# Kernel tuning notes

Measured on AMD Instinct MI355X. Metric: run time of the kernel, lower is better.

## Reference

```python
import jax, jax.numpy as jnp
import numpy as np

B, IN_DIM, K, D = 8192, 1024, 2048, 256
TAU = 1.0
BN_EPS = 1e-5


def setup_inputs() -> dict:
    key = jax.random.key(0)
    ks = jax.random.split(key, 4)
    x = jax.random.normal(ks[0], (B, IN_DIM), dtype=jnp.float32)
    u = jax.random.uniform(ks[1], (B, K), dtype=jnp.float32)  # uniform for gumbel noise
    W = jax.random.normal(ks[2], (IN_DIM, D), dtype=jnp.float32) * 0.02
    b = jnp.zeros((D,), dtype=jnp.float32)
    gamma = jnp.ones((D,), dtype=jnp.float32)
    beta = jnp.zeros((D,), dtype=jnp.float32)
    E = jax.random.normal(ks[3], (K, D), dtype=jnp.float32)  # nn.Embedding default N(0,1)
    return {"x": x, "u": u, "W": W, "b": b, "gamma": gamma, "beta": beta, "E": E}


def reference(x, u, W, b, gamma, beta, E):
    # classifier + BatchNorm1d (training mode: batch stats, biased variance)
    h = x @ W + b                                   # [B, D]
    mu = jnp.mean(h, axis=0)
    var = jnp.var(h, axis=0)
    h = (h - mu) * jax.lax.rsqrt(var + BN_EPS) * gamma + beta
    # negative squared euclidean distance via ||h||^2 - 2 h.E^T + ||e||^2 (GEMM form,
    # avoids materializing [B, K, D])
    h2 = jnp.sum(h * h, axis=-1, keepdims=True)     # [B, 1]
    e2 = jnp.sum(E * E, axis=-1)                    # [K]
    logits = -(h2 - 2.0 * (h @ E.T) + e2)           # [B, K]
    # gumbel-softmax (soft) with tau
    g = -jnp.log(-jnp.log(u + 1e-10) + 1e-10)
    assignments = jax.nn.softmax((logits + g) / TAU, axis=-1)  # [B, K]
    z = assignments @ E                             # [B, D]
    probs = jax.nn.softmax(logits, axis=-1)
    return probs, z
```

## Files before the change

### kernel.cpp

```cpp
#include <hip/hip_runtime.h>
#include <math.h>

#define B_SZ 8192
#define IN_DIM 1024
#define K_CB 2048
#define D_SZ 256
#define BN_EPS 1e-5f

typedef _Float16 f16;
typedef _Float16 f16x8 __attribute__((ext_vector_type(8)));
typedef _Float16 f16x4 __attribute__((ext_vector_type(4)));
typedef float    f32x4 __attribute__((ext_vector_type(4)));

#define GLOAD_LDS16(g, l) __builtin_amdgcn_global_load_lds(                      \
    (const __attribute__((address_space(1))) unsigned int*)(g),                  \
    (__attribute__((address_space(3))) unsigned int*)(l), 16, 0, 0)

template<int BM, int BN, int BK, int EPI, bool A32>
__global__ __launch_bounds__(256) void gemm_mfma(
    const void* __restrict__ Aptr, int lda,
    const f16* __restrict__ Bptr, int ldb,
    void* __restrict__ Cptr, int ldc, int Kdim,
    const float* __restrict__ bias)
{
    constexpr int G    = BK / 8;
    constexpr int MASK = G - 1;
    constexpr int WM = BM / 2, WN = BN / 2;
    constexpr int FM = WM / 16, FN = WN / 16;
    constexpr int CH_A = BM * G;
    constexpr int CH_B = BN * G;

    __shared__ char lds[(BM + BN) * BK * 2];
    char* As = lds;
    char* Bs = lds + BM * BK * 2;

    const int tid  = threadIdx.x;
    const int w    = tid >> 6, lane = tid & 63;
    const int wm   = w >> 1,   wn   = w & 1;
    const int row0 = blockIdx.x * BM;
    const int col0 = blockIdx.y * BN;

    f32x4 acc[FM][FN] = {};

    for (int k0 = 0; k0 < Kdim; k0 += BK) {
        #pragma unroll
        for (int i = 0; i < CH_B / 256; ++i) {
            const int base = (i * 4 + w) * 64;
            const int s = base + lane;
            const int r = s / G, c = s % G;
            const f16* src = Bptr + (size_t)(col0 + r) * ldb + k0 + ((c ^ (r & MASK)) * 8);
            GLOAD_LDS16(src, Bs + base * 16);
        }
        if (!A32) {
            #pragma unroll
            for (int i = 0; i < CH_A / 256; ++i) {
                const int base = (i * 4 + w) * 64;
                const int s = base + lane;
                const int r = s / G, c = s % G;
                const f16* src = (const f16*)Aptr + (size_t)(row0 + r) * lda + k0 + ((c ^ (r & MASK)) * 8);
                GLOAD_LDS16(src, As + base * 16);
            }
        } else {
            #pragma unroll
            for (int i = 0; i < CH_A / 256; ++i) {
                const int s = i * 256 + tid;
                const int r = s / G, c = s % G;
                const float* src = (const float*)Aptr + (size_t)(row0 + r) * lda + k0 + c * 8;
                const float4 v0 = ((const float4*)src)[0];
                const float4 v1 = ((const float4*)src)[1];
                f16x8 d;
                d[0] = (f16)v0.x; d[1] = (f16)v0.y; d[2] = (f16)v0.z; d[3] = (f16)v0.w;
                d[4] = (f16)v1.x; d[5] = (f16)v1.y; d[6] = (f16)v1.z; d[7] = (f16)v1.w;
                *(f16x8*)(As + (r * G + (c ^ (r & MASK))) * 16) = d;
            }
        }
        __syncthreads();

        #pragma unroll
        for (int kk = 0; kk < BK / 32; ++kk) {
            f16x8 af[FM], bf[FN];
            #pragma unroll
            for (int m = 0; m < FM; ++m) {
                const int r = wm * WM + m * 16 + (lane & 15);
                const int g = (kk * 4 + (lane >> 4)) ^ (r & MASK);
                af[m] = *(const f16x8*)(As + r * (BK * 2) + g * 16);
            }
            #pragma unroll
            for (int n = 0; n < FN; ++n) {
                const int r = wn * WN + n * 16 + (lane & 15);
                const int g = (kk * 4 + (lane >> 4)) ^ (r & MASK);
                bf[n] = *(const f16x8*)(Bs + r * (BK * 2) + g * 16);
            }
            #pragma unroll
            for (int m = 0; m < FM; ++m)
                #pragma unroll
                for (int n = 0; n < FN; ++n)
                    acc[m][n] = __builtin_amdgcn_mfma_f32_16x16x32_f16(af[m], bf[n], acc[m][n], 0, 0, 0);
        }
        __syncthreads();
    }

    #pragma unroll
    for (int m = 0; m < FM; ++m) {
        const int rbase = row0 + wm * WM + m * 16 + (lane >> 4) * 4;
        #pragma unroll
        for (int n = 0; n < FN; ++n) {
            const int c = col0 + wn * WN + n * 16 + (lane & 15);
            #pragma unroll
            for (int j = 0; j < 4; ++j) {
                const float v = acc[m][n][j];
                if (EPI == 0) {
                    ((float*)Cptr)[(size_t)(rbase + j) * ldc + c] = v;
                } else {
                    ((f16*)Cptr)[(size_t)(rbase + j) * ldc + c] = (f16)(v + bias[c]);
                }
            }
        }
    }
}

__global__ __launch_bounds__(512, 2) void fused_sm(
    const f16* __restrict__ h16, const f16* __restrict__ E16,
    const float* __restrict__ e2v, const float* __restrict__ u,
    const float* __restrict__ scale, const float* __restrict__ shift,
    float* __restrict__ probs, f16* __restrict__ assign16)
{
    __shared__ __align__(16) char lds_raw[65536];
    f16* Bs = (f16*)lds_raw;
    f16* p1buf = (f16*)lds_raw;
    float* redA = (float*)lds_raw;

    const int tid  = threadIdx.x;
    const int w    = tid >> 6, lane = tid & 63;
    const int q    = lane >> 4, r16 = lane & 15;
    const int row0 = blockIdx.x * 16;
    const int colL = w * 16 + r16;

    f16x8 af[8];
    {
        const f16* hrow = h16 + (size_t)(row0 + r16) * D_SZ + q * 8;
        #pragma unroll
        for (int kk = 0; kk < 8; ++kk) {
            const f16x8 raw = *(const f16x8*)(hrow + kk * 32);
            const float4 scA = *(const float4*)(scale + kk * 32 + q * 8);
            const float4 scB = *(const float4*)(scale + kk * 32 + q * 8 + 4);
            const float4 shA = *(const float4*)(shift + kk * 32 + q * 8);
            const float4 shB = *(const float4*)(shift + kk * 32 + q * 8 + 4);
            f16x8 d;
            d[0] = (f16)fmaf((float)raw[0], scA.x, shA.x);
            d[1] = (f16)fmaf((float)raw[1], scA.y, shA.y);
            d[2] = (f16)fmaf((float)raw[2], scA.z, shA.z);
            d[3] = (f16)fmaf((float)raw[3], scA.w, shA.w);
            d[4] = (f16)fmaf((float)raw[4], scB.x, shB.x);
            d[5] = (f16)fmaf((float)raw[5], scB.y, shB.y);
            d[6] = (f16)fmaf((float)raw[6], scB.z, shB.z);
            d[7] = (f16)fmaf((float)raw[7], scB.w, shB.w);
            af[kk] = d;
        }
    }

    f32x4 acc[16];
    #pragma unroll
    for (int n = 0; n < 16; ++n) acc[n] = (f32x4){0.f, 0.f, 0.f, 0.f};

    #pragma unroll
    for (int c = 0; c < 16; ++c) {
        if (c > 0) __builtin_amdgcn_s_barrier();
        #pragma unroll
        for (int i = 0; i < 8; ++i) {
            const int base = (i * 8 + w) * 64;
            const int s = base + lane;
            const int r = s >> 5, cgg = s & 31;
            GLOAD_LDS16(E16 + (size_t)(c * 128 + r) * D_SZ + ((cgg ^ (r & 31)) * 8),
                        Bs + base * 8);
        }
        asm volatile("s_waitcnt vmcnt(0)" ::: "memory");
        __builtin_amdgcn_s_barrier();
        __builtin_amdgcn_sched_barrier(0);
        #pragma unroll
        for (int kk = 0; kk < 8; ++kk) {
            const int gb = (kk * 4 + q) ^ (colL & 31);
            const f16x8 bf = *(const f16x8*)(Bs + colL * 256 + gb * 8);
            acc[c] = __builtin_amdgcn_mfma_f32_16x16x32_f16(af[kk], bf, acc[c], 0, 0, 0);
        }
        __builtin_amdgcn_sched_barrier(0);
    }
    __syncthreads();

    float m1[4] = {-1e30f, -1e30f, -1e30f, -1e30f};
    #pragma unroll
    for (int n = 0; n < 16; ++n) {
        const float ec = e2v[n * 128 + colL];
        #pragma unroll
        for (int j = 0; j < 4; ++j)
            m1[j] = fmaxf(m1[j], 2.f * acc[n][j] - ec);
    }
    #pragma unroll
    for (int off = 1; off < 16; off <<= 1)
        #pragma unroll
        for (int j = 0; j < 4; ++j)
            m1[j] = fmaxf(m1[j], __shfl_xor(m1[j], off));
    if (r16 == 0)
        #pragma unroll
        for (int j = 0; j < 4; ++j) redA[w * 16 + q * 4 + j] = m1[j];
    __syncthreads();
    #pragma unroll
    for (int j = 0; j < 4; ++j) {
        float a = -1e30f;
        #pragma unroll
        for (int t = 0; t < 8; ++t) a = fmaxf(a, redA[t * 16 + q * 4 + j]);
        m1[j] = a;
    }
    __syncthreads();

    #pragma unroll
    for (int n = 0; n < 16; ++n) {
        const float ec = e2v[n * 128 + colL];
        #pragma unroll
        for (int j = 0; j < 4; ++j) {
            const float lv = 2.f * acc[n][j] - ec;
            p1buf[(q * 4 + j) * 2048 + n * 128 + colL] = (f16)__expf(lv - m1[j] + 10.f);
        }
    }
    __syncthreads();

    const int trow = tid >> 5;
    const int cg   = tid & 31;
    const float* urow = u + (size_t)(row0 + trow) * K_CB + cg * 4;
    const f16* prow_l = p1buf + trow * 2048 + cg * 4;

    float s1 = 0.f, s2 = 0.f;
    f16x4 p1f[16];
    f32x4 t[16];
    #pragma unroll
    for (int n = 0; n < 16; ++n) {
        const float4 u4 = *(const float4*)(urow + n * 128);
        const f16x4 p4 = *(const f16x4*)(prow_l + n * 128);
        const float ua[4] = {u4.x, u4.y, u4.z, u4.w};
        p1f[n] = p4;
        #pragma unroll
        for (int e = 0; e < 4; ++e) {
            const float g = -__logf(-__logf(ua[e] + 1e-10f) + 1e-10f);
            const float te = (float)p4[e] * __expf(g);
            t[n][e] = te;
            s1 += (float)p4[e];
            s2 += te;
        }
    }
    #pragma unroll
    for (int off = 1; off < 32; off <<= 1) {
        s1 += __shfl_xor(s1, off);
        s2 += __shfl_xor(s2, off);
    }
    const float r1 = 1.f / s1;
    const float r2 = 1.f / s2;

    float* prow = probs + (size_t)(row0 + trow) * K_CB + cg * 4;
    f16* arow = assign16 + (size_t)(row0 + trow) * K_CB + cg * 4;
    #pragma unroll
    for (int n = 0; n < 16; ++n) {
        float4 o;
        o.x = (float)p1f[n][0] * r1; o.y = (float)p1f[n][1] * r1;
        o.z = (float)p1f[n][2] * r1; o.w = (float)p1f[n][3] * r1;
        *(float4*)(prow + n * 128) = o;
        f16x4 a4;
        #pragma unroll
        for (int e = 0; e < 4; ++e) a4[e] = (f16)(t[n][e] * r2);
        *(f16x4*)(arow + n * 128) = a4;
    }
}

__global__ __launch_bounds__(256) void conv_WT(const float* __restrict__ W, f16* __restrict__ WT)
{
    const int r = blockIdx.x, c = threadIdx.x;
    WT[c * 1024 + r] = (f16)W[r * 256 + c];
}

__global__ __launch_bounds__(256) void conv_E2(const float* __restrict__ E,
                                               f16* __restrict__ E16, f16* __restrict__ ET,
                                               float* __restrict__ e2)
{
    const int r = blockIdx.x, c = threadIdx.x;
    const int wave = c >> 6, lane = c & 63;
    const float v = E[r * 256 + c];
    E16[r * 256 + c] = (f16)v;
    ET[c * 2048 + r] = (f16)v;
    float ss = v * v;
    #pragma unroll
    for (int off = 32; off > 0; off >>= 1) ss += __shfl_down(ss, off);
    __shared__ float s4[4];
    if (lane == 0) s4[wave] = ss;
    __syncthreads();
    if (c == 0) e2[r] = s4[0] + s4[1] + s4[2] + s4[3];
}

__global__ __launch_bounds__(256) void bn_partial(const f16* __restrict__ h16, float* __restrict__ part)
{
    const int d = threadIdx.x;
    const int blk = blockIdx.x;
    const int r0 = blk * (B_SZ / 128);
    float s = 0.f, sq = 0.f;
    for (int r = r0; r < r0 + (B_SZ / 128); ++r) {
        const float v = (float)h16[(size_t)r * D_SZ + d];
        s += v; sq += v * v;
    }
    part[blk * 512 + d]       = s;
    part[blk * 512 + 256 + d] = sq;
}

__global__ __launch_bounds__(256) void bn_finalize(
    const float* __restrict__ part, const float* __restrict__ gamma, const float* __restrict__ beta,
    float* __restrict__ scale, float* __restrict__ shift)
{
    const int d = threadIdx.x;
    float s = 0.f, sq = 0.f;
    for (int b = 0; b < 128; ++b) { s += part[b * 512 + d]; sq += part[b * 512 + 256 + d]; }
    const float mu  = s / (float)B_SZ;
    const float var = sq / (float)B_SZ - mu * mu;
    const float sc  = gamma[d] * rsqrtf(var + BN_EPS);
    scale[d] = sc;
    shift[d] = beta[d] - mu * sc;
}

extern "C" void kernel_launch(void* const* d_in, const int* in_sizes, int n_in,
                              void* d_out, int out_size, void* d_ws, size_t ws_size,
                              hipStream_t stream)
{
    const float* x     = (const float*)d_in[0];
    const float* u     = (const float*)d_in[1];
    const float* W     = (const float*)d_in[2];
    const float* bias  = (const float*)d_in[3];
    const float* gamma = (const float*)d_in[4];
    const float* beta  = (const float*)d_in[5];
    const float* E     = (const float*)d_in[6];

    float* probs = (float*)d_out;
    float* z     = probs + (size_t)B_SZ * K_CB;

    char* ws = (char*)d_ws;
    f16* assign16 = (f16*)ws;  ws += (size_t)B_SZ * K_CB * 2;
    f16* h16 = (f16*)ws;       ws += (size_t)B_SZ * D_SZ * 2;
    f16* WT16 = (f16*)ws;      ws += (size_t)D_SZ * IN_DIM * 2;
    f16* E16 = (f16*)ws;       ws += (size_t)K_CB * D_SZ * 2;
    f16* ET16 = (f16*)ws;      ws += (size_t)D_SZ * K_CB * 2;
    float* part = (float*)ws;  ws += 128 * 512 * 4;
    float* scale = (float*)ws; ws += D_SZ * 4;
    float* shift = (float*)ws; ws += D_SZ * 4;
    float* e2 = (float*)ws;    ws += K_CB * 4;

    conv_WT<<<IN_DIM, 256, 0, stream>>>(W, WT16);
    conv_E2<<<K_CB, 256, 0, stream>>>(E, E16, ET16, e2);

    {
        dim3 g(B_SZ / 64, D_SZ / 64);
        gemm_mfma<64, 64, 64, 1, true><<<g, 256, 0, stream>>>(
            x, IN_DIM, WT16, IN_DIM, h16, D_SZ, IN_DIM, bias);
    }
    bn_partial<<<128, 256, 0, stream>>>(h16, part);
    bn_finalize<<<1, 256, 0, stream>>>(part, gamma, beta, scale, shift);

    fused_sm<<<B_SZ / 16, 512, 0, stream>>>(h16, E16, e2, u, scale, shift, probs, assign16);

    {
        dim3 g(B_SZ / 64, D_SZ / 64);
        gemm_mfma<64, 64, 128, 0, false><<<g, 256, 0, stream>>>(
            assign16, K_CB, ET16, K_CB, z, D_SZ, K_CB, nullptr);
    }
}
```

Before: 131.0 us.

## Double-buffer codebook tiles and process 32 rows per 1024-thread block

```diff
diff --git a/kernel.cpp b/kernel.cpp
--- a/kernel.cpp
+++ b/kernel.cpp
@@ -119,26 +119,32 @@
     }
 }
 
-__global__ __launch_bounds__(512, 2) void fused_sm(
+#define LP1 2056
+
+__global__ __launch_bounds__(1024, 1) void fused_sm(
     const f16* __restrict__ h16, const f16* __restrict__ E16,
     const float* __restrict__ e2v, const float* __restrict__ u,
     const float* __restrict__ scale, const float* __restrict__ shift,
     float* __restrict__ probs, f16* __restrict__ assign16)
 {
-    __shared__ __align__(16) char lds_raw[65536];
-    f16* Bs = (f16*)lds_raw;
+    __shared__ __align__(16) char lds_raw[32 * LP1 * 2];
+    __shared__ float redA[16 * 16];
+    f16* Bs0 = (f16*)lds_raw;
+    f16* Bs1 = Bs0 + 128 * 256;
     f16* p1buf = (f16*)lds_raw;
-    float* redA = (float*)lds_raw;
 
     const int tid  = threadIdx.x;
     const int w    = tid >> 6, lane = tid & 63;
     const int q    = lane >> 4, r16 = lane & 15;
-    const int row0 = blockIdx.x * 16;
-    const int colL = w * 16 + r16;
+    const int g2   = w >> 3;
+    const int wc   = w & 7;
+    const int row0 = blockIdx.x * 32;
+    const int rowA = row0 + g2 * 16;
+    const int colL = wc * 16 + r16;
 
     f16x8 af[8];
     {
-        const f16* hrow = h16 + (size_t)(row0 + r16) * D_SZ + q * 8;
+        const f16* hrow = h16 + (size_t)(rowA + r16) * D_SZ + q * 8;
         #pragma unroll
         for (int kk = 0; kk < 8; ++kk) {
             const f16x8 raw = *(const f16x8*)(hrow + kk * 32);
@@ -164,25 +170,40 @@
     for (int n = 0; n < 16; ++n) acc[n] = (f32x4){0.f, 0.f, 0.f, 0.f};
 
     #pragma unroll
+    for (int i = 0; i < 4; ++i) {
+        const int base = (i * 16 + w) * 64;
+        const int s = base + lane;
+        const int r = s >> 5, cgg = s & 31;
+        GLOAD_LDS16(E16 + (size_t)r * D_SZ + ((cgg ^ (r & 31)) * 8), Bs0 + base * 8);
+    }
+
+    #pragma unroll
     for (int c = 0; c < 16; ++c) {
-        if (c > 0) __builtin_amdgcn_s_barrier();
-        #pragma unroll
-        for (int i = 0; i < 8; ++i) {
-            const int base = (i * 8 + w) * 64;
-            const int s = base + lane;
-            const int r = s >> 5, cgg = s & 31;
-            GLOAD_LDS16(E16 + (size_t)(c * 128 + r) * D_SZ + ((cgg ^ (r & 31)) * 8),
-                        Bs + base * 8);
-        }
-        asm volatile("s_waitcnt vmcnt(0)" ::: "memory");
+        f16* buf  = (c & 1) ? Bs1 : Bs0;
+        f16* nbuf = (c & 1) ? Bs0 : Bs1;
+        if (c < 15) {
+            #pragma unroll
+            for (int i = 0; i < 4; ++i) {
+                const int base = (i * 16 + w) * 64;
+                const int s = base + lane;
+                const int r = s >> 5, cgg = s & 31;
+                GLOAD_LDS16(E16 + (size_t)((c + 1) * 128 + r) * D_SZ + ((cgg ^ (r & 31)) * 8),
+                            nbuf + base * 8);
+            }
+            asm volatile("s_waitcnt vmcnt(4)" ::: "memory");
+        } else {
+            asm volatile("s_waitcnt vmcnt(0)" ::: "memory");
+        }
         __builtin_amdgcn_s_barrier();
         __builtin_amdgcn_sched_barrier(0);
         #pragma unroll
         for (int kk = 0; kk < 8; ++kk) {
             const int gb = (kk * 4 + q) ^ (colL & 31);
-            const f16x8 bf = *(const f16x8*)(Bs + colL * 256 + gb * 8);
+            const f16x8 bf = *(const f16x8*)(buf + colL * 256 + gb * 8);
             acc[c] = __builtin_amdgcn_mfma_f32_16x16x32_f16(af[kk], bf, acc[c], 0, 0, 0);
         }
+        __builtin_amdgcn_sched_barrier(0);
+        __builtin_amdgcn_s_barrier();
         __builtin_amdgcn_sched_barrier(0);
     }
     __syncthreads();
@@ -208,10 +229,9 @@
     for (int j = 0; j < 4; ++j) {
         float a = -1e30f;
         #pragma unroll
-        for (int t = 0; t < 8; ++t) a = fmaxf(a, redA[t * 16 + q * 4 + j]);
+        for (int t = 0; t < 8; ++t) a = fmaxf(a, redA[(g2 * 8 + t) * 16 + q * 4 + j]);
         m1[j] = a;
     }
-    __syncthreads();
 
     #pragma unroll
     for (int n = 0; n < 16; ++n) {
@@ -219,7 +239,8 @@
         #pragma unroll
         for (int j = 0; j < 4; ++j) {
             const float lv = 2.f * acc[n][j] - ec;
-            p1buf[(q * 4 + j) * 2048 + n * 128 + colL] = (f16)__expf(lv - m1[j] + 10.f);
+            p1buf[(size_t)(g2 * 16 + q * 4 + j) * LP1 + n * 128 + colL] =
+                (f16)__expf(lv - m1[j] + 10.f);
         }
     }
     __syncthreads();
@@ -227,7 +248,7 @@
     const int trow = tid >> 5;
     const int cg   = tid & 31;
     const float* urow = u + (size_t)(row0 + trow) * K_CB + cg * 4;
-    const f16* prow_l = p1buf + trow * 2048 + cg * 4;
+    const f16* prow_l = p1buf + (size_t)trow * LP1 + cg * 4;
 
     float s1 = 0.f, s2 = 0.f;
     f16x4 p1f[16];
@@ -359,7 +380,7 @@
     bn_partial<<<128, 256, 0, stream>>>(h16, part);
     bn_finalize<<<1, 256, 0, stream>>>(part, gamma, beta, scale, shift);
 
-    fused_sm<<<B_SZ / 16, 512, 0, stream>>>(h16, E16, e2, u, scale, shift, probs, assign16);
+    fused_sm<<<B_SZ / 32, 1024, 0, stream>>>(h16, E16, e2, u, scale, shift, probs, assign16);
 
     {
         dim3 g(B_SZ / 64, D_SZ / 64);
```

Measured after the change: 120.9 us. 1.08x faster.

## Split fused softmax kernel into logits-exp and softmax-tail kernels

Applied to the files above, without the earlier changes.

```diff
diff --git a/kernel.cpp b/kernel.cpp
--- a/kernel.cpp
+++ b/kernel.cpp
@@ -119,16 +119,12 @@
     }
 }
 
-__global__ __launch_bounds__(512, 2) void fused_sm(
+__global__ __launch_bounds__(512, 2) void p1gen(
     const f16* __restrict__ h16, const f16* __restrict__ E16,
-    const float* __restrict__ e2v, const float* __restrict__ u,
-    const float* __restrict__ scale, const float* __restrict__ shift,
-    float* __restrict__ probs, f16* __restrict__ assign16)
-{
-    __shared__ __align__(16) char lds_raw[65536];
-    f16* Bs = (f16*)lds_raw;
-    f16* p1buf = (f16*)lds_raw;
-    float* redA = (float*)lds_raw;
+    const float* __restrict__ e2v, const float* __restrict__ scale,
+    const float* __restrict__ shift, f16* __restrict__ p1out)
+{
+    __shared__ float redA[8][16];
 
     const int tid  = threadIdx.x;
     const int w    = tid >> 6, lane = tid & 63;
@@ -164,28 +160,14 @@
     for (int n = 0; n < 16; ++n) acc[n] = (f32x4){0.f, 0.f, 0.f, 0.f};
 
     #pragma unroll
-    for (int c = 0; c < 16; ++c) {
-        if (c > 0) __builtin_amdgcn_s_barrier();
-        #pragma unroll
-        for (int i = 0; i < 8; ++i) {
-            const int base = (i * 8 + w) * 64;
-            const int s = base + lane;
-            const int r = s >> 5, cgg = s & 31;
-            GLOAD_LDS16(E16 + (size_t)(c * 128 + r) * D_SZ + ((cgg ^ (r & 31)) * 8),
-                        Bs + base * 8);
-        }
-        asm volatile("s_waitcnt vmcnt(0)" ::: "memory");
-        __builtin_amdgcn_s_barrier();
-        __builtin_amdgcn_sched_barrier(0);
+    for (int n = 0; n < 16; ++n) {
+        const f16* erow = E16 + (size_t)(n * 128 + colL) * D_SZ + q * 8;
         #pragma unroll
         for (int kk = 0; kk < 8; ++kk) {
-            const int gb = (kk * 4 + q) ^ (colL & 31);
-            const f16x8 bf = *(const f16x8*)(Bs + colL * 256 + gb * 8);
-            acc[c] = __builtin_amdgcn_mfma_f32_16x16x32_f16(af[kk], bf, acc[c], 0, 0, 0);
-        }
-        __builtin_amdgcn_sched_barrier(0);
-    }
-    __syncthreads();
+            const f16x8 bf = *(const f16x8*)(erow + kk * 32);
+            acc[n] = __builtin_amdgcn_mfma_f32_16x16x32_f16(af[kk], bf, acc[n], 0, 0, 0);
+        }
+    }
 
     float m1[4] = {-1e30f, -1e30f, -1e30f, -1e30f};
     #pragma unroll
@@ -202,16 +184,15 @@
             m1[j] = fmaxf(m1[j], __shfl_xor(m1[j], off));
     if (r16 == 0)
         #pragma unroll
-        for (int j = 0; j < 4; ++j) redA[w * 16 + q * 4 + j] = m1[j];
+        for (int j = 0; j < 4; ++j) redA[w][q * 4 + j] = m1[j];
     __syncthreads();
     #pragma unroll
     for (int j = 0; j < 4; ++j) {
         float a = -1e30f;
         #pragma unroll
-        for (int t = 0; t < 8; ++t) a = fmaxf(a, redA[t * 16 + q * 4 + j]);
+        for (int t = 0; t < 8; ++t) a = fmaxf(a, redA[t][q * 4 + j]);
         m1[j] = a;
     }
-    __syncthreads();
 
     #pragma unroll
     for (int n = 0; n < 16; ++n) {
@@ -219,15 +200,24 @@
         #pragma unroll
         for (int j = 0; j < 4; ++j) {
             const float lv = 2.f * acc[n][j] - ec;
-            p1buf[(q * 4 + j) * 2048 + n * 128 + colL] = (f16)__expf(lv - m1[j] + 10.f);
-        }
-    }
-    __syncthreads();
-
+            p1out[(size_t)(row0 + q * 4 + j) * K_CB + n * 128 + colL] =
+                (f16)__expf(lv - m1[j] + 10.f);
+        }
+    }
+}
+
+__global__ __launch_bounds__(512) void smtail(
+    const f16* __restrict__ p1, const float* __restrict__ u,
+    float* __restrict__ probs, f16* __restrict__ assign16)
+{
+    const int tid  = threadIdx.x;
+    const int row0 = blockIdx.x * 16;
     const int trow = tid >> 5;
     const int cg   = tid & 31;
-    const float* urow = u + (size_t)(row0 + trow) * K_CB + cg * 4;
-    const f16* prow_l = p1buf + trow * 2048 + cg * 4;
+    const int row  = row0 + trow;
+
+    const float* urow = u + (size_t)row * K_CB + cg * 4;
+    const f16* prow_l = p1 + (size_t)row * K_CB + cg * 4;
 
     float s1 = 0.f, s2 = 0.f;
     f16x4 p1f[16];
@@ -240,8 +230,8 @@
         p1f[n] = p4;
         #pragma unroll
         for (int e = 0; e < 4; ++e) {
-            const float g = -__logf(-__logf(ua[e] + 1e-10f) + 1e-10f);
-            const float te = (float)p4[e] * __expf(g);
+            const float eg = 1.f / (-__logf(ua[e] + 1e-10f) + 1e-10f);
+            const float te = (float)p4[e] * eg;
             t[n][e] = te;
             s1 += (float)p4[e];
             s2 += te;
@@ -255,8 +245,8 @@
     const float r1 = 1.f / s1;
     const float r2 = 1.f / s2;
 
-    float* prow = probs + (size_t)(row0 + trow) * K_CB + cg * 4;
-    f16* arow = assign16 + (size_t)(row0 + trow) * K_CB + cg * 4;
+    float* prow = probs + (size_t)row * K_CB + cg * 4;
+    f16* arow = assign16 + (size_t)row * K_CB + cg * 4;
     #pragma unroll
     for (int n = 0; n < 16; ++n) {
         float4 o;
@@ -338,6 +328,7 @@
     float* z     = probs + (size_t)B_SZ * K_CB;
 
     char* ws = (char*)d_ws;
+    f16* p1ws = (f16*)ws;      ws += (size_t)B_SZ * K_CB * 2;
     f16* assign16 = (f16*)ws;  ws += (size_t)B_SZ * K_CB * 2;
     f16* h16 = (f16*)ws;       ws += (size_t)B_SZ * D_SZ * 2;
     f16* WT16 = (f16*)ws;      ws += (size_t)D_SZ * IN_DIM * 2;
@@ -359,7 +350,9 @@
     bn_partial<<<128, 256, 0, stream>>>(h16, part);
     bn_finalize<<<1, 256, 0, stream>>>(part, gamma, beta, scale, shift);
 
-    fused_sm<<<B_SZ / 16, 512, 0, stream>>>(h16, E16, e2, u, scale, shift, probs, assign16);
+    p1gen<<<B_SZ / 16, 512, 0, stream>>>(h16, E16, e2, scale, shift, p1ws);
+
+    smtail<<<B_SZ / 16, 512, 0, stream>>>(p1ws, u, probs, assign16);
 
     {
         dim3 g(B_SZ / 64, D_SZ / 64);
```

After: 176.7 us. +34.9%, slower.
